# Kernel tuning notes

Measured on AMD Instinct MI355X. Metric: run time of the kernel, lower is better.

Reference implementation:

```python
import jax, jax.numpy as jnp
import numpy as np

B, S, D_IN, D_OUT, H = 2, 2048, 1024, 1024, 16
HD = D_OUT // H  # 64


def setup_inputs() -> dict:
    key = jax.random.key(0)
    k1, k2, k3, k4 = jax.random.split(key, 4)
    x = jax.random.normal(k1, (B, S, D_IN), dtype=jnp.float32)
    # Linear weights stored pre-transposed as [d_in, d_out] so y = x @ W
    sc = 1.0 / np.sqrt(D_IN)
    Wq = jax.random.normal(k2, (D_IN, D_OUT), dtype=jnp.float32) * sc
    Wk = jax.random.normal(k3, (D_IN, D_OUT), dtype=jnp.float32) * sc
    Wv = jax.random.normal(k4, (D_IN, D_OUT), dtype=jnp.float32) * sc
    return {"x": x, "Wq": Wq, "Wk": Wk, "Wv": Wv}


def reference(x, Wq, Wk, Wv):
    b, s, _ = x.shape
    # project and split heads: [B, S, H, HD]
    q = (x @ Wq).reshape(b, s, H, HD)
    k = (x @ Wk).reshape(b, s, H, HD)
    v = (x @ Wv).reshape(b, s, H, HD)
    # scores: [B, H, Sq, Sk]
    scores = jnp.einsum("bqhd,bkhd->bhqk", q, k)
    # causal mask: triu(ones, diagonal=1) -> mask positions where k > q
    causal = jnp.triu(jnp.ones((s, s), dtype=bool), k=1)
    scores = jnp.where(causal, -jnp.inf, scores)
    # FAITHFUL quirks: scale by sqrt(d_out) (full model dim) and
    # softmax over dim=2 = the QUERY axis of [B, H, Sq, Sk]
    scale = jnp.float32(D_OUT) ** 0.5
    weights = jax.nn.softmax(scores / scale, axis=2)
    # context: [B, H, Sq, HD] -> [B, Sq, H*HD]
    ctx = jnp.einsum("bhqk,bhkd->bhqd", weights, v.transpose(0, 2, 1, 3))
    return ctx.transpose(0, 2, 1, 3).reshape(b, s, H * HD)
```

## Files before the change

### kernel.cpp

```cpp
#include <hip/hip_runtime.h>
#include <hip/hip_bf16.h>


typedef __attribute__((ext_vector_type(8))) short short8;
typedef __attribute__((ext_vector_type(4))) float floatx4;
typedef __attribute__((ext_vector_type(16))) float floatx16;

#define SS 2048
#define DIN 1024
#define DOUT 1024
#define NH 16
#define HD 64
#define QSCALE 0.04508422002778011f

#define MFMA16(a,b,c) __builtin_amdgcn_mfma_f32_16x16x32_bf16((a),(b),(c),0,0,0)
#define MFMA32(a,b,c) __builtin_amdgcn_mfma_f32_32x32x16_bf16((a),(b),(c),0,0,0)
#define EXP2F(x) __builtin_amdgcn_exp2f(x)
#define SBAR() __builtin_amdgcn_s_barrier()
#define WAITV0() asm volatile("s_waitcnt vmcnt(0)" ::: "memory")
#define WAITV4() asm volatile("s_waitcnt vmcnt(4)" ::: "memory")
#define WAITV8() asm volatile("s_waitcnt vmcnt(8)" ::: "memory")

__device__ __forceinline__ void gl_lds16(const void* g, void* l) {
  __builtin_amdgcn_global_load_lds((const __attribute__((address_space(1))) void*)g,
                                   (__attribute__((address_space(3))) void*)l, 16, 0, 0);
}

__device__ __forceinline__ void stage64(const __hip_bfloat16* __restrict__ src, int stride,
                                        __hip_bfloat16* lds, int c, int l) {
  int r = c * 8 + (l >> 3);
  int cc = ((l & 7) ^ ((l >> 3) & 7)) * 8;
  gl_lds16(src + (size_t)r * stride + cc, lds + c * 512);
}

__device__ __forceinline__ short8 frag64(const __hip_bfloat16* lds, int row, int ks, int l) {
  return *(const short8*)&lds[row * 64 + (((ks * 4 + (l >> 4)) ^ (row & 7)) * 8)];
}

__device__ __forceinline__ short8 frag32(const __hip_bfloat16* lds, int row, int subk, int l) {
  return *(const short8*)&lds[row * 64 + (((subk * 2 + (l >> 5)) ^ (row & 7)) * 8)];
}

__global__ __launch_bounds__(256) void k_cvt_x(const float* __restrict__ x,
                                               __hip_bfloat16* __restrict__ xb) {
  size_t i = ((size_t)blockIdx.x * 256 + threadIdx.x) * 4;
  float4 v = *(const float4*)(x + i);
  union { __hip_bfloat16 h[4]; short4 s; } u;
  u.h[0] = __float2bfloat16(v.x); u.h[1] = __float2bfloat16(v.y);
  u.h[2] = __float2bfloat16(v.z); u.h[3] = __float2bfloat16(v.w);
  *(short4*)(xb + i) = u.s;
}

__global__ void k_twb(const float* __restrict__ Wq, const float* __restrict__ Wk,
                      const float* __restrict__ Wv,
                      __hip_bfloat16* __restrict__ wtq, __hip_bfloat16* __restrict__ wtk,
                      __hip_bfloat16* __restrict__ wtv) {
  const float* W; __hip_bfloat16* Wt;
  if (blockIdx.z == 0)      { W = Wq; Wt = wtq; }
  else if (blockIdx.z == 1) { W = Wk; Wt = wtk; }
  else                      { W = Wv; Wt = wtv; }
  __shared__ float t[32][33];
  int tx = threadIdx.x, ty = threadIdx.y;
  int k0 = blockIdx.y * 32, c0 = blockIdx.x * 32;
#pragma unroll
  for (int i = 0; i < 4; ++i)
    t[ty + 8*i][tx] = W[(size_t)(k0 + ty + 8*i) * DOUT + c0 + tx];
  __syncthreads();
#pragma unroll
  for (int i = 0; i < 4; ++i)
    Wt[(size_t)(c0 + ty + 8*i) * DIN + k0 + tx] = __float2bfloat16(t[tx][ty + 8*i]);
}

__global__ __launch_bounds__(256) void k_qkv(
    const __hip_bfloat16* __restrict__ xb,
    const __hip_bfloat16* __restrict__ wq, const __hip_bfloat16* __restrict__ wk,
    const __hip_bfloat16* __restrict__ wv,
    __hip_bfloat16* __restrict__ qb, __hip_bfloat16* __restrict__ kb,
    __hip_bfloat16* __restrict__ vb) {
  __shared__ __hip_bfloat16 smem[32768];

  const __hip_bfloat16* wt; __hip_bfloat16* outp;
  if (blockIdx.z == 0)      { wt = wq; outp = qb; }
  else if (blockIdx.z == 1) { wt = wk; outp = kb; }
  else                      { wt = wv; outp = vb; }

  const int tid = threadIdx.x, w = tid >> 6, l = tid & 63;
  const int row0 = blockIdx.y * 128, col0 = blockIdx.x * 128;
  const int mw = (w >> 1) * 64, nw = (w & 1) * 64;

  const floatx4 fz = {0.f, 0.f, 0.f, 0.f};
  floatx4 acc[4][4];
#pragma unroll
  for (int m = 0; m < 4; ++m)
#pragma unroll
    for (int n = 0; n < 4; ++n) acc[m][n] = fz;

#pragma unroll
  for (int i = 0; i < 4; ++i) {
    stage64(xb + (size_t)row0 * DIN, DIN, smem, w*4+i, l);
    stage64(wt + (size_t)col0 * DIN, DIN, smem + 16384, w*4+i, l);
  }

  for (int kt = 0; kt < 16; ++kt) {
    int cur = kt & 1;
    __hip_bfloat16* Ac = smem + cur * 8192;
    __hip_bfloat16* Bc = smem + 16384 + cur * 8192;
    if (kt < 15) {
      int kk = (kt + 1) * 64;
      __hip_bfloat16* An = smem + (cur ^ 1) * 8192;
      __hip_bfloat16* Bn = smem + 16384 + (cur ^ 1) * 8192;
#pragma unroll
      for (int i = 0; i < 4; ++i) {
        stage64(xb + (size_t)row0 * DIN + kk, DIN, An, w*4+i, l);
        stage64(wt + (size_t)col0 * DIN + kk, DIN, Bn, w*4+i, l);
      }
      WAITV8();
    } else {
      WAITV0();
    }
    SBAR();
    short8 a[4][2], b[4][2];
#pragma unroll
    for (int m = 0; m < 4; ++m)
#pragma unroll
      for (int ks = 0; ks < 2; ++ks)
        a[m][ks] = frag64(Ac, mw + m*16 + (l & 15), ks, l);
#pragma unroll
    for (int n = 0; n < 4; ++n)
#pragma unroll
      for (int ks = 0; ks < 2; ++ks)
        b[n][ks] = frag64(Bc, nw + n*16 + (l & 15), ks, l);
#pragma unroll
    for (int ks = 0; ks < 2; ++ks)
#pragma unroll
      for (int m = 0; m < 4; ++m)
#pragma unroll
        for (int n = 0; n < 4; ++n)
          acc[m][n] = MFMA16(a[m][ks], b[n][ks], acc[m][n]);
    SBAR();
  }

  int bb2 = row0 >> 11, sbase = row0 & (SS - 1);
  if (blockIdx.z == 2) {
    __hip_bfloat16* Vt2 = smem;
#pragma unroll
    for (int m = 0; m < 4; ++m)
#pragma unroll
      for (int n = 0; n < 4; ++n)
#pragma unroll
        for (int r4 = 0; r4 < 4; ++r4) {
          int r = mw + m*16 + ((l >> 4) << 2) + r4;
          int c = nw + n*16 + (l & 15);
          Vt2[c * 136 + r] = __float2bfloat16(acc[m][n][r4]);
        }
    __syncthreads();
#pragma unroll
    for (int i = 0; i < 8; ++i) {
      int drow = (tid >> 4) + i * 16;
      int scol = (tid & 15) * 8;
      int colg = col0 + drow, hh = colg >> 6, d = colg & 63;
      *(short8*)(outp + (((size_t)bb2 * NH + hh) * HD + d) * SS + sbase + scol) =
          *(const short8*)&Vt2[drow * 136 + scol];
    }
  } else {
    float sc = (blockIdx.z == 0) ? QSCALE : 1.0f;
    __hip_bfloat16* T2 = smem;
#pragma unroll
    for (int m = 0; m < 4; ++m)
#pragma unroll
      for (int n = 0; n < 4; ++n)
#pragma unroll
        for (int r4 = 0; r4 < 4; ++r4) {
          int r = mw + m*16 + ((l >> 4) << 2) + r4;
          int c = nw + n*16 + (l & 15);
          T2[r * 136 + c] = __float2bfloat16(acc[m][n][r4] * sc);
        }
    __syncthreads();
#pragma unroll
    for (int i = 0; i < 8; ++i) {
      int r = (tid >> 4) + i * 16;
      int c = (tid & 15) * 8;
      int colg = col0 + c, hh = colg >> 6, d = colg & 63;
      *(short8*)(outp + (((size_t)bb2 * NH + hh) * SS + sbase + r) * HD + d) =
          *(const short8*)&T2[r * 136 + c];
    }
  }
}

__global__ __launch_bounds__(256) void k_cstat(const __hip_bfloat16* __restrict__ qb,
                                               const __hip_bfloat16* __restrict__ kb,
                                               __hip_bfloat16* __restrict__ vtb) {
  __shared__ __hip_bfloat16 smem[20480];
  __shared__ float red[4][64];
  __shared__ float zl[64];
  __hip_bfloat16* Kt = smem;
  const int bh = blockIdx.x;
  const int j = blockIdx.y;
  const int tid = threadIdx.x, w = tid >> 6, l = tid & 63;
  const int k0 = j * 64;
  const int t0 = j >> 1, niter = 16 - t0;

#pragma unroll
  for (int i = 0; i < 2; ++i)
    stage64(kb + ((size_t)bh * SS + k0) * HD, HD, Kt, w*2+i, l);
#pragma unroll
  for (int i = 0; i < 4; ++i)
    stage64(qb + ((size_t)bh * SS + (t0 << 7)) * HD, HD, smem + 4096, w*4+i, l);

  short8 kf[4][2];
  float csum[4] = {0.f, 0.f, 0.f, 0.f};
  for (int it = 0; it < niter; ++it) {
    int cur = it & 1;
    __hip_bfloat16* Qc = smem + 4096 + cur * 8192;
    int q0 = (t0 + it) << 7;
    if (it + 1 < niter) {
      __hip_bfloat16* Qn = smem + 4096 + (cur ^ 1) * 8192;
#pragma unroll
      for (int i = 0; i < 4; ++i)
        stage64(qb + ((size_t)bh * SS + q0 + 128) * HD, HD, Qn, w*4+i, l);
      WAITV4();
    } else {
      WAITV0();
    }
    SBAR();
    if (it == 0) {
#pragma unroll
      for (int n = 0; n < 4; ++n)
#pragma unroll
        for (int ks = 0; ks < 2; ++ks)
          kf[n][ks] = frag64(Kt, n*16 + (l & 15), ks, l);
    }
    int qw = q0 + w * 32;
    if (qw + 31 >= k0) {
      short8 qa[2][2];
#pragma unroll
      for (int mm = 0; mm < 2; ++mm)
#pragma unroll
        for (int ks = 0; ks < 2; ++ks)
          qa[mm][ks] = frag64(Qc, w*32 + mm*16 + (l & 15), ks, l);
      floatx4 s[2][4];
#pragma unroll
      for (int mm = 0; mm < 2; ++mm)
#pragma unroll
        for (int n = 0; n < 4; ++n) {
          floatx4 t = {0.f, 0.f, 0.f, 0.f};
#pragma unroll
          for (int ks = 0; ks < 2; ++ks) t = MFMA16(qa[mm][ks], kf[n][ks], t);
          s[mm][n] = t;
        }
      bool dia = (k0 + 63 > qw);
#pragma unroll
      for (int mm = 0; mm < 2; ++mm)
#pragma unroll
        for (int n = 0; n < 4; ++n)
#pragma unroll
          for (int r4 = 0; r4 < 4; ++r4) {
            float e = EXP2F(s[mm][n][r4]);
            if (dia) {
              int q = qw + mm*16 + ((l >> 4) << 2) + r4;
              int k = k0 + n*16 + (l & 15);
              if (k > q) e = 0.f;
            }
            csum[n] += e;
          }
    }
    SBAR();
  }

#pragma unroll
  for (int n = 0; n < 4; ++n) {
    csum[n] += __shfl_xor(csum[n], 16);
    csum[n] += __shfl_xor(csum[n], 32);
    if (l < 16) red[w][n*16 + l] = csum[n];
  }
  __syncthreads();
  if (tid < 64)
    zl[tid] = 1.0f / (red[0][tid] + red[1][tid] + red[2][tid] + red[3][tid]);
  __syncthreads();
#pragma unroll
  for (int i = 0; i < 4; ++i) {
    int d = (tid >> 4) + i * 16;
    int c = (tid & 15) * 4;
    size_t base = ((size_t)bh * HD + d) * SS + k0 + c;
    short4 v = *(const short4*)(vtb + base);
    __hip_bfloat16* hp = (__hip_bfloat16*)&v;
#pragma unroll
    for (int jv = 0; jv < 4; ++jv)
      hp[jv] = __float2bfloat16(__bfloat162float(hp[jv]) * zl[c + jv]);
    *(short4*)(vtb + base) = v;
  }
}

__global__ __launch_bounds__(1024, 4) void k_ctx(const __hip_bfloat16* __restrict__ qb,
                                                 const __hip_bfloat16* __restrict__ kb,
                                                 const __hip_bfloat16* __restrict__ vtb,
                                                 float* __restrict__ outp) {
  __shared__ __hip_bfloat16 smem[65536];
  const int i = blockIdx.x;
  const int bh = i & 31, bb = bh >> 4, h = bh & 15;
  const int tb = (i < 256) ? (15 - (i >> 5)) : ((i - 256) >> 5);
  const int Q0 = tb * 128;
  const int tid = threadIdx.x, w = tid >> 6, l = tid & 63;
  const int g = w & 3, s = w >> 2;
  const int hi = l >> 5;
  const int qg = Q0 + g + 4 * (l & 31);
  const int nkt = 2 * (tb + 1);
  const int nit = (nkt + 3) >> 2;
  __hip_bfloat16* qsm = smem + s * 16384;

  short8 qf[4];
  {
    const __hip_bfloat16* qrow = qb + ((size_t)bh * SS + qg) * HD + hi * 8;
#pragma unroll
    for (int hc = 0; hc < 4; ++hc)
      qf[hc] = *(const short8*)(qrow + hc * 16);
  }
  asm volatile("" :: "v"(qf[0]), "v"(qf[1]), "v"(qf[2]), "v"(qf[3]));
  WAITV0();

  if (s < nkt) {
    int kn = s << 6;
#pragma unroll
    for (int ii = 0; ii < 2; ++ii) {
      stage64(kb + ((size_t)bh * SS + kn) * HD, HD, qsm, g*2+ii, l);
      stage64(vtb + (size_t)bh * HD * SS + kn, SS, qsm + 8192, g*2+ii, l);
    }
  }

  const floatx16 fz16 = {0,0,0,0,0,0,0,0,0,0,0,0,0,0,0,0};
  floatx16 acc[2];
  acc[0] = fz16; acc[1] = fz16;

  for (int it = 0; it < nit; ++it) {
    int cur = it & 1;
    __hip_bfloat16* Kc = qsm + cur * 4096;
    __hip_bfloat16* Vc = qsm + 8192 + cur * 4096;
    const int myk = s + 4 * it;
    const int nxt = myk + 4;
    if (nxt < nkt) {
      int kn = nxt << 6;
#pragma unroll
      for (int ii = 0; ii < 2; ++ii) {
        stage64(kb + ((size_t)bh * SS + kn) * HD, HD, qsm + (cur^1) * 4096, g*2+ii, l);
        stage64(vtb + (size_t)bh * HD * SS + kn, SS, qsm + 8192 + (cur^1) * 4096, g*2+ii, l);
      }
      WAITV4();
    } else {
      WAITV0();
    }
    SBAR();

    if (myk < nkt) {
      const int k0 = myk << 6;
      floatx16 st[2];
#pragma unroll
      for (int H = 0; H < 2; ++H) {
        floatx16 t = fz16;
#pragma unroll
        for (int hc = 0; hc < 4; ++hc)
          t = MFMA32(frag32(Kc, H*32 + (l & 31), hc, l), qf[hc], t);
        st[H] = t;
      }
      const bool dia = (k0 + 63 > Q0 + g);
      unsigned pk[2][4][2];
#pragma unroll
      for (int H = 0; H < 2; ++H)
#pragma unroll
        for (int m = 0; m < 4; ++m)
#pragma unroll
          for (int pr = 0; pr < 2; ++pr) {
            float e0 = EXP2F(st[H][m*4 + pr*2]);
            float e1 = EXP2F(st[H][m*4 + pr*2 + 1]);
            if (dia) {
              int kb0 = k0 + H*32 + m*8 + hi*4 + pr*2;
              if (kb0 > qg)     e0 = 0.f;
              if (kb0 + 1 > qg) e1 = 0.f;
            }
            pk[H][m][pr] = (unsigned)__bfloat16_as_ushort(__float2bfloat16(e0)) |
                           ((unsigned)__bfloat16_as_ushort(__float2bfloat16(e1)) << 16);
          }
#pragma unroll
      for (int ks = 0; ks < 4; ++ks) {
        const int H = ks >> 1, mb = (ks & 1) * 2;
        unsigned keep0 = hi ? pk[H][mb+1][0] : pk[H][mb][0];
        unsigned keep1 = hi ? pk[H][mb+1][1] : pk[H][mb][1];
        unsigned send0 = hi ? pk[H][mb][0]   : pk[H][mb+1][0];
        unsigned send1 = hi ? pk[H][mb][1]   : pk[H][mb+1][1];
        unsigned recv0 = (unsigned)__shfl_xor((int)send0, 32);
        unsigned recv1 = (unsigned)__shfl_xor((int)send1, 32);
        union { unsigned u[4]; short8 sv; } pa;
        pa.u[0] = hi ? recv0 : keep0;
        pa.u[1] = hi ? recv1 : keep1;
        pa.u[2] = hi ? keep0 : recv0;
        pa.u[3] = hi ? keep1 : recv1;
#pragma unroll
        for (int dn = 0; dn < 2; ++dn)
          acc[dn] = MFMA32(pa.sv, frag32(Vc, dn*32 + (l & 31), ks, l), acc[dn]);
      }
    }
    SBAR();
  }

  float* fsm = (float*)smem;
  if (s > 0) {
    float* dst = fsm + ((s - 1) * 4 + g) * 2048;
#pragma unroll
    for (int dn = 0; dn < 2; ++dn)
#pragma unroll
      for (int r = 0; r < 16; ++r)
        dst[(dn * 16 + r) * 64 + l] = acc[dn][r];
  }
  __syncthreads();
  if (s == 0) {
#pragma unroll
    for (int sp = 0; sp < 3; ++sp) {
      const float* src = fsm + (sp * 4 + g) * 2048;
#pragma unroll
      for (int dn = 0; dn < 2; ++dn)
#pragma unroll
        for (int r = 0; r < 16; ++r)
          acc[dn][r] += src[(dn * 16 + r) * 64 + l];
    }
#pragma unroll
    for (int dn = 0; dn < 2; ++dn)
#pragma unroll
      for (int r = 0; r < 16; ++r) {
        int q = Q0 + g + 4 * ((r & 3) + 8*(r >> 2) + 4*hi);
        outp[((size_t)bb * SS + q) * DOUT + h * HD + dn*32 + (l & 31)] = acc[dn][r];
      }
  }
}

extern "C" void kernel_launch(void* const* d_in, const int* in_sizes, int n_in,
                              void* d_out, int out_size, void* d_ws, size_t ws_size,
                              hipStream_t stream) {
  const float* x  = (const float*)d_in[0];
  const float* Wq = (const float*)d_in[1];
  const float* Wk = (const float*)d_in[2];
  const float* Wv = (const float*)d_in[3];
  float* out = (float*)d_out;
  char* ws = (char*)d_ws;

  __hip_bfloat16* xb  = (__hip_bfloat16*)(ws);
  __hip_bfloat16* wtq = (__hip_bfloat16*)(ws + (8ull  << 20));
  __hip_bfloat16* wtk = (__hip_bfloat16*)(ws + (10ull << 20));
  __hip_bfloat16* wtv = (__hip_bfloat16*)(ws + (12ull << 20));
  __hip_bfloat16* qb  = (__hip_bfloat16*)(ws + (14ull << 20));
  __hip_bfloat16* kb  = (__hip_bfloat16*)(ws + (22ull << 20));
  __hip_bfloat16* vtb = (__hip_bfloat16*)(ws + (30ull << 20));

  k_cvt_x<<<4096, 256, 0, stream>>>(x, xb);
  dim3 tb(32, 8);
  k_twb<<<dim3(32, 32, 3), tb, 0, stream>>>(Wq, Wk, Wv, wtq, wtk, wtv);
  k_qkv<<<dim3(8, 32, 3), 256, 0, stream>>>(xb, wtq, wtk, wtv, qb, kb, vtb);
  k_cstat<<<dim3(32, 32), 256, 0, stream>>>(qb, kb, vtb);
  k_ctx<<<dim3(512), 1024, 0, stream>>>(qb, kb, vtb, out);
}
```

Baseline: 114.7 us.

## Halve k_ctx block to two key-splits and use dual MFMA accumulators

The context kernel block drops from 16 waves (4 key-split groups) to 8 waves (2 key-split groups). Each group now walks every other key tile, and shared memory and the cross-split reduction shrink to match. The QK and PV MFMA chains are split into two independent accumulators to break dependency latency. This means fewer partial sums to reduce, more blocks per CU and no idle splits on small causal tiles, at the cost of longer per-wave serial loops.

Result: slower. 242.0 us (+111.0%).

```diff
diff --git a/kernel.cpp b/kernel.cpp
--- a/kernel.cpp
+++ b/kernel.cpp
@@ -291,11 +291,11 @@
   }
 }
 
-__global__ __launch_bounds__(1024, 4) void k_ctx(const __hip_bfloat16* __restrict__ qb,
-                                                 const __hip_bfloat16* __restrict__ kb,
-                                                 const __hip_bfloat16* __restrict__ vtb,
-                                                 float* __restrict__ outp) {
-  __shared__ __hip_bfloat16 smem[65536];
+__global__ __launch_bounds__(512, 4) void k_ctx(const __hip_bfloat16* __restrict__ qb,
+                                                const __hip_bfloat16* __restrict__ kb,
+                                                const __hip_bfloat16* __restrict__ vtb,
+                                                float* __restrict__ outp) {
+  __shared__ __hip_bfloat16 smem[32768];
   const int i = blockIdx.x;
   const int bh = i & 31, bb = bh >> 4, h = bh & 15;
   const int tb = (i < 256) ? (15 - (i >> 5)) : ((i - 256) >> 5);
@@ -305,7 +305,7 @@
   const int hi = l >> 5;
   const int qg = Q0 + g + 4 * (l & 31);
   const int nkt = 2 * (tb + 1);
-  const int nit = (nkt + 3) >> 2;
+  const int nit = nkt >> 1;
   __hip_bfloat16* qsm = smem + s * 16384;
 
   short8 qf[4];
@@ -318,7 +318,7 @@
   asm volatile("" :: "v"(qf[0]), "v"(qf[1]), "v"(qf[2]), "v"(qf[3]));
   WAITV0();
 
-  if (s < nkt) {
+  {
     int kn = s << 6;
 #pragma unroll
     for (int ii = 0; ii < 2; ++ii) {
@@ -328,15 +328,15 @@
   }
 
   const floatx16 fz16 = {0,0,0,0,0,0,0,0,0,0,0,0,0,0,0,0};
-  floatx16 acc[2];
-  acc[0] = fz16; acc[1] = fz16;
+  floatx16 accA[2], accB[2];
+  accA[0] = fz16; accA[1] = fz16; accB[0] = fz16; accB[1] = fz16;
 
   for (int it = 0; it < nit; ++it) {
     int cur = it & 1;
     __hip_bfloat16* Kc = qsm + cur * 4096;
     __hip_bfloat16* Vc = qsm + 8192 + cur * 4096;
-    const int myk = s + 4 * it;
-    const int nxt = myk + 4;
+    const int myk = s + 2 * it;
+    const int nxt = myk + 2;
     if (nxt < nkt) {
       int kn = nxt << 6;
 #pragma unroll
@@ -350,16 +350,17 @@
     }
     SBAR();
 
-    if (myk < nkt) {
+    {
       const int k0 = myk << 6;
       floatx16 st[2];
 #pragma unroll
       for (int H = 0; H < 2; ++H) {
-        floatx16 t = fz16;
-#pragma unroll
-        for (int hc = 0; hc < 4; ++hc)
-          t = MFMA32(frag32(Kc, H*32 + (l & 31), hc, l), qf[hc], t);
-        st[H] = t;
+        floatx16 tA = fz16, tB = fz16;
+        tA = MFMA32(frag32(Kc, H*32 + (l & 31), 0, l), qf[0], tA);
+        tB = MFMA32(frag32(Kc, H*32 + (l & 31), 1, l), qf[1], tB);
+        tA = MFMA32(frag32(Kc, H*32 + (l & 31), 2, l), qf[2], tA);
+        tB = MFMA32(frag32(Kc, H*32 + (l & 31), 3, l), qf[3], tB);
+        st[H] = tA + tB;
       }
       const bool dia = (k0 + 63 > Q0 + g);
       unsigned pk[2][4][2];
@@ -393,17 +394,27 @@
         pa.u[1] = hi ? recv1 : keep1;
         pa.u[2] = hi ? keep0 : recv0;
         pa.u[3] = hi ? keep1 : recv1;
-#pragma unroll
-        for (int dn = 0; dn < 2; ++dn)
-          acc[dn] = MFMA32(pa.sv, frag32(Vc, dn*32 + (l & 31), ks, l), acc[dn]);
+        if (ks < 2) {
+#pragma unroll
+          for (int dn = 0; dn < 2; ++dn)
+            accA[dn] = MFMA32(pa.sv, frag32(Vc, dn*32 + (l & 31), ks, l), accA[dn]);
+        } else {
+#pragma unroll
+          for (int dn = 0; dn < 2; ++dn)
+            accB[dn] = MFMA32(pa.sv, frag32(Vc, dn*32 + (l & 31), ks, l), accB[dn]);
+        }
       }
     }
     SBAR();
   }
 
+  floatx16 acc[2];
+  acc[0] = accA[0] + accB[0];
+  acc[1] = accA[1] + accB[1];
+
   float* fsm = (float*)smem;
-  if (s > 0) {
-    float* dst = fsm + ((s - 1) * 4 + g) * 2048;
+  if (s == 1) {
+    float* dst = fsm + g * 2048;
 #pragma unroll
     for (int dn = 0; dn < 2; ++dn)
 #pragma unroll
@@ -412,15 +423,12 @@
   }
   __syncthreads();
   if (s == 0) {
-#pragma unroll
-    for (int sp = 0; sp < 3; ++sp) {
-      const float* src = fsm + (sp * 4 + g) * 2048;
-#pragma unroll
-      for (int dn = 0; dn < 2; ++dn)
-#pragma unroll
-        for (int r = 0; r < 16; ++r)
-          acc[dn][r] += src[(dn * 16 + r) * 64 + l];
-    }
+    const float* src = fsm + g * 2048;
+#pragma unroll
+    for (int dn = 0; dn < 2; ++dn)
+#pragma unroll
+      for (int r = 0; r < 16; ++r)
+        acc[dn][r] += src[(dn * 16 + r) * 64 + l];
 #pragma unroll
     for (int dn = 0; dn < 2; ++dn)
 #pragma unroll
@@ -454,5 +462,5 @@
   k_twb<<<dim3(32, 32, 3), tb, 0, stream>>>(Wq, Wk, Wv, wtq, wtk, wtv);
   k_qkv<<<dim3(8, 32, 3), 256, 0, stream>>>(xb, wtq, wtk, wtv, qb, kb, vtb);
   k_cstat<<<dim3(32, 32), 256, 0, stream>>>(qb, kb, vtb);
-  k_ctx<<<dim3(512), 1024, 0, stream>>>(qb, kb, vtb, out);
-}
+  k_ctx<<<dim3(512), 512, 0, stream>>>(qb, kb, vtb, out);
+}
```
